# Optimization experiments

Measured on AMD Instinct MI355X. Metric: run time of the kernel, lower is better.

The kernel has to match this reference:

```python
import jax, jax.numpy as jnp
import numpy as np

M_CENTER = 3.0  # diagonal value of the 'centers' matrix
OUT_HW = (513, 513)  # original input spatial size (input_shape in torch forward)


def _conv(x, w, dilation=1, padding=0):
    return jax.lax.conv_general_dilated(
        x, w, window_strides=(1, 1),
        padding=[(padding, padding), (padding, padding)],
        rhs_dilation=(dilation, dilation),
        dimension_numbers=("NCHW", "OIHW", "NCHW"))


def _resize(x, hw):
    return jax.image.resize(x, (x.shape[0], x.shape[1], hw[0], hw[1]), method="bilinear")


def _head(low_level, out, pw, w0, w1, w2, w3, pool_w, aproj_w, cw1, cw2, cb2):
    # DeepLabHeadV3Plus (BN folded to identity at inference: gamma=1, beta=0, mean=0, var=1)
    ll = jax.nn.relu(_conv(low_level, pw))                      # [N,48,129,129]
    branches = [jax.nn.relu(_conv(out, w0))]                    # 1x1 branch
    for w, d in zip((w1, w2, w3), (6, 12, 18)):
        branches.append(jax.nn.relu(_conv(out, w, dilation=d, padding=d)))
    gp = jnp.mean(out, axis=(2, 3), keepdims=True)              # AdaptiveAvgPool2d(1)
    gp = jax.nn.relu(_conv(gp, pool_w))
    gp = jnp.broadcast_to(gp, branches[0].shape)                # bilinear upsample of 1x1 == broadcast
    branches.append(gp)
    y = jax.nn.relu(_conv(jnp.concatenate(branches, axis=1), aproj_w))  # [N,256,33,33]
    y = _resize(y, (ll.shape[2], ll.shape[3]))                  # -> 129x129
    y = jnp.concatenate([ll, y], axis=1)                        # [N,304,129,129]
    y = jax.nn.relu(_conv(y, cw1, padding=1))
    y = _conv(y, cw2) + cb2[None, :, None, None]                # [N,C,129,129]
    return y


def _forward_single(x):
    # x: [N,C,129,129] head logits. Upsample, then squared-distance to diagonal centers (m*I).
    x = _resize(x, OUT_HW)                                      # [N,C,513,513]
    C = x.shape[1]
    features_out = jnp.transpose(x, (0, 2, 3, 1))               # NHWC, as in torch
    # dist2mean[...,c] = -sum_j (f_j - m*1[j==c])^2 = -(|f|^2 - 2*m*f_c + m^2)
    sumsq = jnp.sum(x * x, axis=1, keepdims=True)
    logits = 2.0 * M_CENTER * x - sumsq - M_CENTER * M_CENTER   # [N,C,513,513]
    centers = M_CENTER * jnp.eye(C, dtype=x.dtype)
    return logits, centers, features_out


def _kaiming(key, shape):
    fan_in = shape[1] * shape[2] * shape[3]
    return jax.random.normal(key, shape, jnp.float32) * np.sqrt(2.0 / fan_in)


def _head_params(key, num_classes):
    ks = jax.random.split(key, 10)
    return dict(
        pw=_kaiming(ks[0], (48, 256, 1, 1)),
        w0=_kaiming(ks[1], (256, 2048, 1, 1)),
        w1=_kaiming(ks[2], (256, 2048, 3, 3)),
        w2=_kaiming(ks[3], (256, 2048, 3, 3)),
        w3=_kaiming(ks[4], (256, 2048, 3, 3)),
        pool_w=_kaiming(ks[5], (256, 2048, 1, 1)),
        aproj_w=_kaiming(ks[6], (256, 1280, 1, 1)),
        cw1=_kaiming(ks[7], (256, 304, 3, 3)),
        cw2=_kaiming(ks[8], (num_classes, 256, 1, 1)),
        cb2=jnp.zeros((num_classes,), jnp.float32),
    )


def setup_inputs() -> dict:
    key = jax.random.key(0)
    k_ll, k_out, k_h0, k_h1 = jax.random.split(key, 4)
    inp = {
        "low_level": jax.random.normal(k_ll, (2, 256, 129, 129), jnp.float32),
        "out": jax.random.normal(k_out, (2, 2048, 33, 33), jnp.float32),
    }
    for pref, k, nc in (("h0_", k_h0, 16), ("h1_", k_h1, 17)):
        for name, v in _head_params(k, nc).items():
            inp[pref + name] = v
    return inp


def reference(low_level, out,
              h0_pw, h0_w0, h0_w1, h0_w2, h0_w3, h0_pool_w, h0_aproj_w, h0_cw1, h0_cw2, h0_cb2,
              h1_pw, h1_w0, h1_w1, h1_w2, h1_w3, h1_pool_w, h1_aproj_w, h1_cw1, h1_cw2, h1_cb2):
    x0 = _head(low_level, out, h0_pw, h0_w0, h0_w1, h0_w2, h0_w3, h0_pool_w, h0_aproj_w, h0_cw1, h0_cw2, h0_cb2)
    x1 = _head(low_level, out, h1_pw, h1_w0, h1_w1, h1_w2, h1_w3, h1_pool_w, h1_aproj_w, h1_cw1, h1_cw2, h1_cb2)
    l0, c0, f0 = _forward_single(x0)
    l1, c1, f1 = _forward_single(x1)
    return (l0, l1, c0, c1, f0, f1)
```

## Files before the change

kernel.cpp:

```cpp
#include <hip/hip_runtime.h>

#define TPB 256

typedef _Float16 f16;
typedef __attribute__((ext_vector_type(8))) _Float16 f16x8;
typedef __attribute__((ext_vector_type(16))) float f32x16;

#define GLD_LDS(g, l) __builtin_amdgcn_global_load_lds( \
    (const __attribute__((address_space(1))) void*)(g), \
    (__attribute__((address_space(3))) void*)(l), 16, 0, 0)

__global__ __launch_bounds__(TPB)
void tcz_k(const float* __restrict__ aspp, const float* __restrict__ ll,
           f16* __restrict__ Xa, f16* __restrict__ Xll)
{
    const int bid = blockIdx.x;
    const int tid = threadIdx.x;
    const float* src; f16* dst; int C, HW, ldk, pT, cT, bb;
    if (bid < 4480) {
        src = aspp; dst = Xa; C = 2048; HW = 1089; ldk = 2048;
        pT = bid % 35; cT = (bid / 35) % 64; bb = bid / 2240;
    } else {
        const int b2 = bid - 4480;
        src = ll; dst = Xll; C = 256; HW = 16641; ldk = 256;
        pT = b2 % 521; cT = (b2 / 521) % 8; bb = b2 / 4168;
    }
    __shared__ float t32[32 * 33];
#pragma unroll
    for (int pass = 0; pass < 4; ++pass) {
        const int ch = tid / 32 + pass * 8;
        const int px = tid % 32;
        const int c = cT * 32 + ch, p = pT * 32 + px;
        float v = 0.f;
        if (c < C && p < HW) v = src[((long)bb * C + c) * HW + p];
        t32[ch * 33 + px] = v;
    }
    __syncthreads();
#pragma unroll
    for (int pass = 0; pass < 4; ++pass) {
        const int px = tid / 32 + pass * 8;
        const int ch = tid % 32;
        const int p = pT * 32 + px, c = cT * 32 + ch;
        if (p < HW && c < C)
            dst[((long)bb * HW + p) * ldk + c] = (f16)t32[ch * 33 + px];
    }
}

__global__ __launch_bounds__(TPB)
void tcr_k(const f16* __restrict__ part, f16* __restrict__ dst)
{
    __shared__ float t32[32 * 33];
    const int pT = blockIdx.x, cT = blockIdx.y, bb = blockIdx.z;
    const int tid = threadIdx.x;
    const int br = cT >> 3;
    const f16* pb = part + (long)bb * 2787840;
#pragma unroll
    for (int pass = 0; pass < 4; ++pass) {
        const int ch = tid / 32 + pass * 8;
        const int px = tid % 32;
        const int c = cT * 32 + ch;
        const int cl = c & 255;
        const int p = pT * 32 + px;
        float v = 0.f;
        if (p < 1089) {
            if (br == 0) {
                v = (float)pb[(long)cl * 1089 + p];
            } else {
                const int dl = 6 * br;
                const int y = p / 33;
                const int s0 = 1 + 3 * (br - 1);
#pragma unroll
                for (int g = 0; g < 3; ++g) {
                    const int dy0 = (g - 1) * dl;
                    const int yLo = max(0, -dy0), yHi = min(33, 33 - dy0);
                    if (y >= yLo && y < yHi)
                        v += (float)pb[((long)(s0 + g) * 256 + cl) * 1089 + p];
                }
            }
            v = fmaxf(v, 0.f);
        }
        t32[ch * 33 + px] = v;
    }
    __syncthreads();
#pragma unroll
    for (int pass = 0; pass < 4; ++pass) {
        const int px = tid / 32 + pass * 8;
        const int ch = tid % 32;
        const int p = pT * 32 + px, c = cT * 32 + ch;
        if (p < 1089)
            dst[((long)bb * 1089 + p) * 1024 + c] = (f16)t32[ch * 33 + px];
    }
}

__global__ __launch_bounds__(TPB)
void gpool_k(const float* __restrict__ in, float* __restrict__ gp, int HW, float inv)
{
    const int bc = blockIdx.x;
    const float* p = in + (size_t)bc * HW;
    float s = 0.f;
    for (int i = threadIdx.x; i < HW; i += TPB) s += p[i];
#pragma unroll
    for (int off = 32; off > 0; off >>= 1) s += __shfl_down(s, off, 64);
    __shared__ float red[4];
    if ((threadIdx.x & 63) == 0) red[threadIdx.x >> 6] = s;
    __syncthreads();
    if (threadIdx.x == 0) gp[bc] = (red[0] + red[1] + red[2] + red[3]) * inv;
}

__global__ __launch_bounds__(TPB)
void gemv1_k(const float* __restrict__ pw0, const float* __restrict__ pw1,
             const float* __restrict__ gp, float* __restrict__ gpr2)
{
    const int bh = blockIdx.x & 3;
    const int cgrp = blockIdx.x >> 2;
    const int b = bh & 1;
    const float* w = (bh >> 1) ? pw1 : pw0;
    const int c = cgrp * 16 + (threadIdx.x >> 4);
    const int kl = threadIdx.x & 15;
    const float* g = gp + (size_t)b * 2048;
    float4 acc = {0.f, 0.f, 0.f, 0.f};
    for (int k = kl * 4; k < 2048; k += 64) {
        const float4 wv = *(const float4*)&w[(size_t)c * 2048 + k];
        const float4 gv = *(const float4*)&g[k];
        acc.x = fmaf(wv.x, gv.x, acc.x);
        acc.y = fmaf(wv.y, gv.y, acc.y);
        acc.z = fmaf(wv.z, gv.z, acc.z);
        acc.w = fmaf(wv.w, gv.w, acc.w);
    }
    float s = (acc.x + acc.y) + (acc.z + acc.w);
#pragma unroll
    for (int o = 8; o; o >>= 1) s += __shfl_xor(s, o, 16);
    if (kl == 0) gpr2[bh * 256 + c] = fmaxf(s, 0.f);
}

__global__ __launch_bounds__(TPB)
void gemv2_k(const float* __restrict__ ap0, const float* __restrict__ ap1,
             const float* __restrict__ gpr2, float* __restrict__ gpc2)
{
    const int bh = blockIdx.x & 3;
    const int cgrp = blockIdx.x >> 2;
    const float* w = (bh >> 1) ? ap1 : ap0;
    const int c = cgrp * 16 + (threadIdx.x >> 4);
    const int kl = threadIdx.x & 15;
    const float* g = gpr2 + bh * 256;
    float4 acc = {0.f, 0.f, 0.f, 0.f};
    for (int k = kl * 4; k < 256; k += 64) {
        const float4 wv = *(const float4*)&w[(size_t)c * 1280 + 1024 + k];
        const float4 gv = *(const float4*)&g[k];
        acc.x = fmaf(wv.x, gv.x, acc.x);
        acc.y = fmaf(wv.y, gv.y, acc.y);
        acc.z = fmaf(wv.z, gv.z, acc.z);
        acc.w = fmaf(wv.w, gv.w, acc.w);
    }
    float s = (acc.x + acc.y) + (acc.z + acc.w);
#pragma unroll
    for (int o = 8; o; o >>= 1) s += __shfl_xor(s, o, 16);
    if (kl == 0) gpc2[bh * 256 + c] = s;
}

struct PackJob { const float* w; f16* dst; int Cout, CinUse, CinSrc, T, coP, KB, start; };
struct PackParams { PackJob j[14]; };

__global__ __launch_bounds__(TPB)
void packw_mega(PackParams P, float* __restrict__ guard)
{
    const int bid = blockIdx.x;
    const int tid = threadIdx.x;
    if (bid >= 4832) {
        float4 zv = {0.f, 0.f, 0.f, 0.f};
        float4* p = (float4*)(guard + tid * 16);
        p[0] = zv; p[1] = zv; p[2] = zv; p[3] = zv;
        return;
    }
    int ji = 0;
#pragma unroll
    for (int t = 1; t < 14; ++t) if (bid >= P.j[t].start) ji = t;
    PackJob J;
    switch (ji) {
        case 0:  J = P.j[0];  break;
        case 1:  J = P.j[1];  break;
        case 2:  J = P.j[2];  break;
        case 3:  J = P.j[3];  break;
        case 4:  J = P.j[4];  break;
        case 5:  J = P.j[5];  break;
        case 6:  J = P.j[6];  break;
        case 7:  J = P.j[7];  break;
        case 8:  J = P.j[8];  break;
        case 9:  J = P.j[9];  break;
        case 10: J = P.j[10]; break;
        case 11: J = P.j[11]; break;
        case 12: J = P.j[12]; break;
        default: J = P.j[13]; break;
    }
    const int local = bid - J.start;
    const int kb = local % J.KB;
    const int coT = local / J.KB;
    const int T = J.T;
    __shared__ float tile[16 * 577];
    const int RL = 64 * T;
    const int n = 16 * RL;
    for (int idx = tid; idx < n; idx += TPB) {
        const int row = idx / RL;
        const int jj = idx - row * RL;
        const int co = coT * 16 + row;
        const int k = kb * 64 + jj / T;
        float v = 0.f;
        if (co < J.Cout && k < J.CinUse)
            v = J.w[((long)co * J.CinSrc + kb * 64) * T + jj];
        tile[row * 577 + jj] = v;
    }
    __syncthreads();
    const int nst = 128 * T;
    for (int idx = tid; idx < nst; idx += TPB) {
        const int g = idx & 7;
        const int t = (idx >> 3) % T;
        const int co = idx / (8 * T);
        f16x8 hv;
#pragma unroll
        for (int e = 0; e < 8; ++e)
            hv[e] = (f16)tile[co * 577 + (g * 8 + e) * T + t];
        *(f16x8*)&J.dst[(((long)t * J.KB + kb) * J.coP + coT * 16 + co) * 64 + g * 8] = hv;
    }
}

template <int OUTMODE, int ZMAP, int RELUOUT, int BIAS>
__global__ __launch_bounds__(TPB, 4)
void mconv(const f16* __restrict__ X, const f16* __restrict__ Wp,
           const f16* __restrict__ guard, void* __restrict__ out_,
           const float* __restrict__ gpc,
           int Cinp, int Cout, int H, int W, int kss_, int dl_,
           int kbPerTap, int tapCnt_,
           long xHstr, long wHstr, long oHstr, long outBStride,
           int coP, int ldOut, int NM, int NBH, int NZ)
{
    __shared__ char SH[32768];
    const int tid = threadIdx.x;

    int wg;
    {
        const int orig = blockIdx.x, nwg = gridDim.x;
        const int q = nwg >> 3, r = nwg & 7;
        const int xcd = orig & 7, off = orig >> 3;
        wg = (xcd < r ? xcd * (q + 1) : r * (q + 1) + (xcd - r) * q) + off;
    }
    const int mt = wg % NM; wg /= NM;
    const int bh = wg % NBH; wg /= NBH;
    const int z  = wg % NZ;
    const int nt = wg / NZ;
    const int b = bh & 1, hd = bh >> 1;
    const int co0 = mt * 128;
    const int NP = H * W;
    const long xBstr = (long)NP * Cinp;

    int kss = kss_, dl = dl_, tapStart = 0, tapCnt = tapCnt_;
    long woff = (long)hd * wHstr, ooff = (long)hd * oHstr;
    int p0 = nt * 128, pMax = NP;
    if (ZMAP == 1) {
        int br, grp;
        if (z == 0) { br = 0; grp = 1; kss = 1; dl = 1; tapStart = 0; tapCnt = 1; }
        else { br = 1 + (z - 1) / 3; grp = (z - 1) % 3;
               kss = 3; dl = (br == 1) ? 6 : (br == 2 ? 12 : 18);
               tapStart = grp * 3; tapCnt = 3; }
        woff += (br == 0) ? 0L : (br == 1 ? 524288L : (br == 2 ? 5242880L : 9961472L));
        ooff += (long)z * 278784L;
        const int dy0 = (kss == 1) ? 0 : (grp - 1) * dl;
        const int yLo = max(0, -dy0), yHi = min(H, H - dy0);
        p0 = yLo * W + nt * 128;
        pMax = yHi * W;
        if (p0 >= pMax) return;
    }
    const int half = kss >> 1;
    const int y0t = p0 / W, y1t = min(p0 + 127, pMax - 1) / W;

    int taps[9]; int nval = 0;
    for (int t = 0; t < tapCnt; ++t) {
        const int tp = tapStart + t;
        const int ky = tp / kss;
        const int dy = (ky - half) * dl;
        if (ZMAP == 1 || (y1t + dy >= 0 && y0t + dy < H)) taps[nval++] = tp;
    }
    if (nval == 0) return;

    const int srow = tid >> 3;
    const int sslot = tid & 7;
    int aofs[4];
#pragma unroll
    for (int q = 0; q < 4; ++q) {
        const int row = q * 32 + srow;
        aofs[q] = row * 64 + ((sslot ^ (row & 7)) << 3);
    }
    const long coStr = (long)coP * 64;

    const int lane = tid & 63, wid = tid >> 6;
    const int wm = wid >> 1, wn = wid & 1;
    const int r32 = lane & 31, hh = lane >> 5;
    const int arow0 = wm * 64 + r32, arow1 = arow0 + 32;
    const int brow0 = wn * 64 + r32, brow1 = brow0 + 32;
    const int abase0 = arow0 * 128, abase1 = arow1 * 128;
    const int bbase0 = 16384 + brow0 * 128, bbase1 = 16384 + brow1 * 128;
    const int ax0 = (arow0 & 7), ax1 = (arow1 & 7);
    const int bx0 = (brow0 & 7), bx1 = (brow1 & 7);

    f32x16 acc[2][2];
#pragma unroll
    for (int i = 0; i < 2; ++i)
#pragma unroll
        for (int j = 0; j < 2; ++j) acc[i][j] = (f32x16)(0.f);

    const f16* Pr[4];
    for (int ti = 0; ti < nval; ++ti) {
        const int tp = taps[ti];
        const int ky = tp / kss, kx = tp - ky * kss;
        const int dy = (ky - half) * dl, dx = (kx - half) * dl;
#pragma unroll
        for (int q = 0; q < 4; ++q) {
            const int row = q * 32 + srow;
            const int p = p0 + row;
            bool v = p < pMax;
            const int py = v ? p / W : 0;
            const int px = v ? p - py * W : 0;
            const int sy = py + dy, sx = px + dx;
            v = v && ((unsigned)sy < (unsigned)H) && ((unsigned)sx < (unsigned)W);
            const int swz = (sslot ^ (row & 7)) << 3;
            Pr[q] = v ? (X + (long)b * xBstr + (long)hd * xHstr
                           + ((long)sy * W + sx) * (long)Cinp + swz)
                      : (guard + swz);
        }
        const f16* Wt = Wp + woff + ((long)tp * kbPerTap * coP + (long)co0) * 64;
        for (int kb = 0; kb < kbPerTap; ++kb) {
            __syncthreads();
            const f16* wsrc = Wt + (long)kb * coStr;
            const long kcol = (long)kb << 6;
            GLD_LDS(wsrc + aofs[0], SH + (tid << 4));
            GLD_LDS(wsrc + aofs[1], SH + 4096 + (tid << 4));
            GLD_LDS(wsrc + aofs[2], SH + 8192 + (tid << 4));
            GLD_LDS(wsrc + aofs[3], SH + 12288 + (tid << 4));
            GLD_LDS(Pr[0] + kcol, SH + 16384 + (tid << 4));
            GLD_LDS(Pr[1] + kcol, SH + 20480 + (tid << 4));
            GLD_LDS(Pr[2] + kcol, SH + 24576 + (tid << 4));
            GLD_LDS(Pr[3] + kcol, SH + 28672 + (tid << 4));
            __syncthreads();
            __builtin_amdgcn_s_setprio(1);
#pragma unroll
            for (int kh = 0; kh < 4; ++kh) {
                const int g = kh * 2 + hh;
                const f16x8 a0 = *(const f16x8*)(SH + abase0 + ((g ^ ax0) << 4));
                const f16x8 a1 = *(const f16x8*)(SH + abase1 + ((g ^ ax1) << 4));
                const f16x8 b0 = *(const f16x8*)(SH + bbase0 + ((g ^ bx0) << 4));
                const f16x8 b1 = *(const f16x8*)(SH + bbase1 + ((g ^ bx1) << 4));
                acc[0][0] = __builtin_amdgcn_mfma_f32_32x32x16_f16(a0, b0, acc[0][0], 0, 0, 0);
                acc[0][1] = __builtin_amdgcn_mfma_f32_32x32x16_f16(a0, b1, acc[0][1], 0, 0, 0);
                acc[1][0] = __builtin_amdgcn_mfma_f32_32x32x16_f16(a1, b0, acc[1][0], 0, 0, 0);
                acc[1][1] = __builtin_amdgcn_mfma_f32_32x32x16_f16(a1, b1, acc[1][1], 0, 0, 0);
            }
            __builtin_amdgcn_s_setprio(0);
        }
    }

    const long outB = (long)b * outBStride + ooff;
    const float* gpcp = BIAS ? (gpc + (long)(b + 2 * hd) * 256) : nullptr;
#pragma unroll
    for (int mi = 0; mi < 2; ++mi)
#pragma unroll
    for (int ni = 0; ni < 2; ++ni)
#pragma unroll
    for (int j = 0; j < 16; ++j) {
        const int m = wm * 64 + mi * 32 + 4 * hh + (j & 3) + 8 * (j >> 2);
        const int n = wn * 64 + ni * 32 + r32;
        const int co = co0 + m;
        const int p = p0 + n;
        if (co < Cout && p < pMax) {
            float v = acc[mi][ni][j];
            if (BIAS) v += gpcp[co];
            if (RELUOUT) v = fmaxf(v, 0.f);
            if (OUTMODE == 0)      ((float*)out_)[outB + (long)co * NP + p] = v;
            else if (OUTMODE == 1) ((f16*)out_)[outB + (long)co * NP + p] = (f16)v;
            else if (OUTMODE == 3) ((f16*)out_)[outB + (long)p * ldOut + co] = (f16)v;
            else atomicAdd(&((float*)out_)[outB + (long)co * NP + p], v);
        }
    }
}

__global__ __launch_bounds__(TPB)
void ups2pad_k(const f16* __restrict__ ybx, f16* __restrict__ ccx)
{
    const int idx = blockIdx.x * TPB + threadIdx.x;
    if (idx >= 4 * 16641 * 34) return;
    const int s = idx / (16641 * 34);
    const int rem = idx - s * (16641 * 34);
    const int p = rem / 34;
    const int cg = rem - p * 34;
    if (cg >= 32) {
        f16x8 zv = (f16x8)(f16)0.f;
        *(f16x8*)(ccx + ((long)s * 16641 + p) * 320 + 304 + (cg - 32) * 8) = zv;
        return;
    }
    const int oy = p / 129, ox = p % 129;
    const float sc = 33.0f / 129.0f;
    const float sx = (ox + 0.5f) * sc - 0.5f;
    const float sy = (oy + 0.5f) * sc - 0.5f;
    int ix0 = (int)floorf(sx), iy0 = (int)floorf(sy);
    const float fx = sx - ix0, fy = sy - iy0;
    int ix1 = min(32, max(0, ix0 + 1)); ix0 = min(32, max(0, ix0));
    int iy1 = min(32, max(0, iy0 + 1)); iy0 = min(32, max(0, iy0));
    const f16* base = ybx + (long)s * 1089 * 256 + cg * 8;
    const f16x8 v00 = *(const f16x8*)(base + ((long)iy0 * 33 + ix0) * 256);
    const f16x8 v01 = *(const f16x8*)(base + ((long)iy0 * 33 + ix1) * 256);
    const f16x8 v10 = *(const f16x8*)(base + ((long)iy1 * 33 + ix0) * 256);
    const f16x8 v11 = *(const f16x8*)(base + ((long)iy1 * 33 + ix1) * 256);
    f16x8 r;
#pragma unroll
    for (int e = 0; e < 8; ++e) {
        const float a0 = (float)v00[e] + ((float)v01[e] - (float)v00[e]) * fx;
        const float a1 = (float)v10[e] + ((float)v11[e] - (float)v10[e]) * fx;
        r[e] = (f16)(a0 + (a1 - a0) * fy);
    }
    *(f16x8*)(ccx + ((long)s * 16641 + p) * 320 + 48 + cg * 8) = r;
}

__global__ __launch_bounds__(TPB)
void conv1x1_m(const f16* __restrict__ c1o2,
               const float* __restrict__ w0, const float* __restrict__ w1,
               const float* __restrict__ b0, const float* __restrict__ b1,
               float* __restrict__ xb2)
{
    const int h = blockIdx.z;
    const int nc = h ? 17 : 16;
    const float* w = h ? w1 : w0;
    const float* bias = h ? b1 : b0;
    __shared__ float wsm[256 * 17];
    __shared__ float bsm[17];
    const int tid = threadIdx.x;
    for (int l = tid; l < 256 * 17; l += TPB) {
        const int k = l / 17, c = l - k * 17;
        wsm[l] = (c < nc) ? w[(size_t)c * 256 + k] : 0.f;
    }
    if (tid < nc) bsm[tid] = bias[tid];
    __syncthreads();
    const int b = blockIdx.y;
    const int p = blockIdx.x * TPB + tid;
    if (p >= 16641) return;
    const f16* inB = c1o2 + (long)h * 8520192 + (long)b * 4260096 + p;
    float acc[17];
#pragma unroll
    for (int c = 0; c < 17; ++c) acc[c] = 0.f;
    for (int k = 0; k < 256; ++k) {
        const float x = (float)inB[(size_t)k * 16641];
#pragma unroll
        for (int c = 0; c < 17; ++c) acc[c] = fmaf(wsm[k * 17 + c], x, acc[c]);
    }
    float* oB = xb2 + (h ? 532512L : 0L) + ((long)b * nc) * 16641 + p;
#pragma unroll
    for (int c = 0; c < 17; ++c)
        if (c < nc) oB[(size_t)c * 16641] = acc[c] + bsm[c];
}

__global__ __launch_bounds__(TPB)
void final_m(const float* __restrict__ xb2, float* __restrict__ o)
{
    const int idx = blockIdx.x * TPB + threadIdx.x;
    if (idx >= 2 * 526338) return;
    const int hd = idx / 526338;
    int r = idx - hd * 526338;
    const int ox = r % 513; r /= 513;
    const int oy = r % 513;
    const int b = r / 513;
    const int nc = hd ? 17 : 16;
    const long HW = 513L * 513L;
    const float sc = 129.0f / 513.0f;
    const float sx = (ox + 0.5f) * sc - 0.5f;
    const float sy = (oy + 0.5f) * sc - 0.5f;
    int ix0 = (int)floorf(sx), iy0 = (int)floorf(sy);
    const float fx = sx - ix0, fy = sy - iy0;
    int ix1 = min(128, max(0, ix0 + 1)); ix0 = min(128, max(0, ix0));
    int iy1 = min(128, max(0, iy0 + 1)); iy0 = min(128, max(0, iy0));
    const float* xb = xb2 + (hd ? 532512L : 0L) + (size_t)b * nc * 16641;
    const int i00 = iy0 * 129 + ix0, i01 = iy0 * 129 + ix1;
    const int i10 = iy1 * 129 + ix0, i11 = iy1 * 129 + ix1;
    float* logits = o + (hd ? 8421408L : 0L);
    float* feats  = o + (hd ? 25791107L : 17369699L);
    float v[17];
    float ss = 0.f;
#pragma unroll
    for (int c = 0; c < 17; ++c) {
        if (c < nc) {
            const float* s = xb + (size_t)c * 16641;
            const float a0 = s[i00] + (s[i01] - s[i00]) * fx;
            const float a1 = s[i10] + (s[i11] - s[i10]) * fx;
            const float vv = a0 + (a1 - a0) * fy;
            v[c] = vv;
            ss = fmaf(vv, vv, ss);
        }
    }
    const long pix = (long)oy * 513 + ox;
#pragma unroll
    for (int c = 0; c < 17; ++c)
        if (c < nc)
            logits[((size_t)b * nc + c) * HW + pix] = fmaf(6.f, v[c], -ss - 9.f);
    float* f = feats + ((size_t)b * HW + pix) * nc;
#pragma unroll
    for (int c = 0; c < 17; ++c)
        if (c < nc) f[c] = v[c];
}

__global__ void centers_k(float* __restrict__ c0, float* __restrict__ c1)
{
    const int t = blockIdx.x * 64 + threadIdx.x;
    if (t < 256) c0[t] = (t / 16 == t % 16) ? 3.f : 0.f;
    const int u = t - 256;
    if (u >= 0 && u < 289) c1[u] = (u / 17 == u % 17) ? 3.f : 0.f;
}

extern "C" void kernel_launch(void* const* d_in, const int* in_sizes, int n_in,
                              void* d_out, int out_size, void* d_ws, size_t ws_size,
                              hipStream_t stream)
{
    const float* low_level = (const float*)d_in[0];
    const float* aspp_in   = (const float*)d_in[1];
    float* ws = (float*)d_ws;
    float* o  = (float*)d_out;

    float* GUARDF  = ws + 0;
    f16*   GUARD   = (f16*)GUARDF;
    f16*   Apack2  = (f16*)(ws + 4096);
    f16*   C1O2    = (f16*)(ws + 4096);
    f16*   AprojP2 = (f16*)(ws + 14684160);
    f16*   Cw1P2   = (f16*)(ws + 14946304);
    f16*   LlP2    = (f16*)(ws + 15683584);
    f16*   Xa      = (f16*)(ws + 15716352);
    f16*   BRpart  = (f16*)(ws + 17946624);
    f16*   BRX2    = (f16*)(ws + 23522304);
    f16*   YBX2    = (f16*)(ws + 25752576);
    float* XB2     = ws + 26310144;
    float* GP      = ws + 27408450;
    float* GPC2    = ws + 27412546;
    float* GPR2    = ws + 27413570;

    f16*   CCX2    = (f16*)(o + 0);
    f16*   Xll     = (f16*)(o + 10650240);

    const long C0o = 17369154, C1oo = 17369410;

    tcz_k<<<12816, TPB, 0, stream>>>(aspp_in, low_level, Xa, Xll);
    gpool_k<<<4096, TPB, 0, stream>>>(aspp_in, GP, 1089, 1.0f / 1089.0f);
    gemv1_k<<<64, TPB, 0, stream>>>(
        (const float*)d_in[2 + 5], (const float*)d_in[2 + 10 + 5], GP, GPR2);
    gemv2_k<<<64, TPB, 0, stream>>>(
        (const float*)d_in[2 + 6], (const float*)d_in[2 + 10 + 6], GPR2, GPC2);

    PackParams P;
    int start = 0;
    for (int h = 0; h < 2; ++h) {
        const float* pw    = (const float*)d_in[2 + h * 10 + 0];
        const float* w0    = (const float*)d_in[2 + h * 10 + 1];
        const float* w1    = (const float*)d_in[2 + h * 10 + 2];
        const float* w2    = (const float*)d_in[2 + h * 10 + 3];
        const float* w3    = (const float*)d_in[2 + h * 10 + 4];
        const float* aproj = (const float*)d_in[2 + h * 10 + 6];
        const float* cw1   = (const float*)d_in[2 + h * 10 + 7];
        f16* Ap = Apack2 + (long)h * 14680064;
        const PackJob jobs[7] = {
            { w0,    Ap,                          256, 2048, 2048, 1, 256, 32, 0 },
            { w1,    Ap + 524288,                 256, 2048, 2048, 9, 256, 32, 0 },
            { w2,    Ap + 5242880,                256, 2048, 2048, 9, 256, 32, 0 },
            { w3,    Ap + 9961472,                256, 2048, 2048, 9, 256, 32, 0 },
            { aproj, AprojP2 + (long)h * 262144,  256, 1024, 1280, 1, 256, 16, 0 },
            { cw1,   Cw1P2 + (long)h * 737280,    256,  304,  304, 9, 256,  5, 0 },
            { pw,    LlP2 + (long)h * 32768,       48,  256,  256, 1, 128,  4, 0 },
        };
        for (int t = 0; t < 7; ++t) {
            P.j[h * 7 + t] = jobs[t];
            P.j[h * 7 + t].start = start;
            start += jobs[t].KB * (jobs[t].coP / 16);
        }
    }
    packw_mega<<<4833, TPB, 0, stream>>>(P, GUARDF);

    mconv<1, 1, 0, 0><<<720, TPB, 0, stream>>>(
        Xa, Apack2, GUARD, BRpart, nullptr, 2048, 256, 33, 33, 3, 1,
        32, 0, 0L, 14680064L, 5575680L, 2787840L, 256, 0, 2, 4, 10);
    tcr_k<<<dim3(35, 32, 4), TPB, 0, stream>>>(BRpart, BRX2);
    mconv<3, 0, 1, 1><<<72, TPB, 0, stream>>>(
        BRX2, AprojP2, GUARD, YBX2, GPC2, 1024, 256, 33, 33, 1, 1,
        16, 1, 2230272L, 262144L, 557568L, 278784L, 256, 256, 2, 4, 1);
    mconv<3, 0, 1, 0><<<524, TPB, 0, stream>>>(
        Xll, LlP2, GUARD, CCX2, nullptr, 256, 48, 129, 129, 1, 1,
        4, 1, 0L, 32768L, 10650240L, 5325120L, 128, 320, 1, 4, 1);
    ups2pad_k<<<8841, TPB, 0, stream>>>(YBX2, CCX2);
    mconv<1, 0, 1, 0><<<1048, TPB, 0, stream>>>(
        CCX2, Cw1P2, GUARD, C1O2, nullptr, 320, 256, 129, 129, 3, 1,
        5, 9, 10650240L, 737280L, 8520192L, 4260096L, 256, 0, 2, 4, 1);
    conv1x1_m<<<dim3(66, 2, 2), TPB, 0, stream>>>(C1O2,
        (const float*)d_in[2 + 8], (const float*)d_in[2 + 10 + 8],
        (const float*)d_in[2 + 9], (const float*)d_in[2 + 10 + 9], XB2);
    final_m<<<4113, TPB, 0, stream>>>(XB2, o);
    centers_k<<<9, 64, 0, stream>>>(o + C0o, o + C1oo);
}
```

Before: 637.6 us.

## Split ASPP conv per tap, fuse low-level 1x1 conv and global pool into launches

The dilated ASPP convolution is now split by individual tap (28 z-slices instead of 10), so each workgroup runs 32 K-blocks instead of 96. The low-level 1x1 projection conv is merged into the same launch, and the global-average-pool reduction is folded into the transpose kernel, removing two launches. The aim is more parallelism and fewer launches. The cost is that the partial-sum buffer grows about threefold (moved into the output region) and tcr_k now has to read and sum nine partials per branch instead of three.

```diff
diff --git a/kernel.cpp b/kernel.cpp
--- a/kernel.cpp
+++ b/kernel.cpp
@@ -12,10 +12,24 @@
 
 __global__ __launch_bounds__(TPB)
 void tcz_k(const float* __restrict__ aspp, const float* __restrict__ ll,
-           f16* __restrict__ Xa, f16* __restrict__ Xll)
+           f16* __restrict__ Xa, f16* __restrict__ Xll, float* __restrict__ gp)
 {
     const int bid = blockIdx.x;
     const int tid = threadIdx.x;
+    __shared__ float t32[32 * 33];
+    __shared__ float red[4];
+    if (bid >= 12816) {
+        const int bc = bid - 12816;
+        const float* p = aspp + (size_t)bc * 1089;
+        float s = 0.f;
+        for (int i = tid; i < 1089; i += TPB) s += p[i];
+#pragma unroll
+        for (int off = 32; off > 0; off >>= 1) s += __shfl_down(s, off, 64);
+        if ((tid & 63) == 0) red[tid >> 6] = s;
+        __syncthreads();
+        if (tid == 0) gp[bc] = (red[0] + red[1] + red[2] + red[3]) * (1.0f / 1089.0f);
+        return;
+    }
     const float* src; f16* dst; int C, HW, ldk, pT, cT, bb;
     if (bid < 4480) {
         src = aspp; dst = Xa; C = 2048; HW = 1089; ldk = 2048;
@@ -25,7 +39,6 @@
         src = ll; dst = Xll; C = 256; HW = 16641; ldk = 256;
         pT = b2 % 521; cT = (b2 / 521) % 8; bb = b2 / 4168;
     }
-    __shared__ float t32[32 * 33];
 #pragma unroll
     for (int pass = 0; pass < 4; ++pass) {
         const int ch = tid / 32 + pass * 8;
@@ -53,7 +66,7 @@
     const int pT = blockIdx.x, cT = blockIdx.y, bb = blockIdx.z;
     const int tid = threadIdx.x;
     const int br = cT >> 3;
-    const f16* pb = part + (long)bb * 2787840;
+    const f16* pb = part + (long)bb * 7806464;
 #pragma unroll
     for (int pass = 0; pass < 4; ++pass) {
         const int ch = tid / 32 + pass * 8;
@@ -67,14 +80,14 @@
                 v = (float)pb[(long)cl * 1089 + p];
             } else {
                 const int dl = 6 * br;
+                const int s0 = 1 + 9 * (br - 1);
                 const int y = p / 33;
-                const int s0 = 1 + 3 * (br - 1);
-#pragma unroll
-                for (int g = 0; g < 3; ++g) {
-                    const int dy0 = (g - 1) * dl;
-                    const int yLo = max(0, -dy0), yHi = min(33, 33 - dy0);
+#pragma unroll
+                for (int t = 0; t < 9; ++t) {
+                    const int dy = (t / 3 - 1) * dl;
+                    const int yLo = max(0, -dy), yHi = min(33, 33 - dy);
                     if (y >= yLo && y < yHi)
-                        v += (float)pb[((long)(s0 + g) * 256 + cl) * 1089 + p];
+                        v += (float)pb[((long)(s0 + t) * 256 + cl) * 1089 + p];
                 }
             }
             v = fmaxf(v, 0.f);
@@ -90,21 +103,6 @@
         if (p < 1089)
             dst[((long)bb * 1089 + p) * 1024 + c] = (f16)t32[ch * 33 + px];
     }
-}
-
-__global__ __launch_bounds__(TPB)
-void gpool_k(const float* __restrict__ in, float* __restrict__ gp, int HW, float inv)
-{
-    const int bc = blockIdx.x;
-    const float* p = in + (size_t)bc * HW;
-    float s = 0.f;
-    for (int i = threadIdx.x; i < HW; i += TPB) s += p[i];
-#pragma unroll
-    for (int off = 32; off > 0; off >>= 1) s += __shfl_down(s, off, 64);
-    __shared__ float red[4];
-    if ((threadIdx.x & 63) == 0) red[threadIdx.x >> 6] = s;
-    __syncthreads();
-    if (threadIdx.x == 0) gp[bc] = (red[0] + red[1] + red[2] + red[3]) * inv;
 }
 
 __global__ __launch_bounds__(TPB)
@@ -223,15 +221,11 @@
     }
 }
 
-template <int OUTMODE, int ZMAP, int RELUOUT, int BIAS>
 __global__ __launch_bounds__(TPB, 4)
-void mconv(const f16* __restrict__ X, const f16* __restrict__ Wp,
-           const f16* __restrict__ guard, void* __restrict__ out_,
-           const float* __restrict__ gpc,
-           int Cinp, int Cout, int H, int W, int kss_, int dl_,
-           int kbPerTap, int tapCnt_,
-           long xHstr, long wHstr, long oHstr, long outBStride,
-           int coP, int ldOut, int NM, int NBH, int NZ)
+void mconv2_k(const f16* __restrict__ Xa, const f16* __restrict__ Xll,
+              const f16* __restrict__ Wa, const f16* __restrict__ Wl,
+              const f16* __restrict__ guard, f16* __restrict__ brp,
+              f16* __restrict__ ccx)
 {
     __shared__ char SH[32768];
     const int tid = threadIdx.x;
@@ -243,41 +237,182 @@
         const int xcd = orig & 7, off = orig >> 3;
         wg = (xcd < r ? xcd * (q + 1) : r * (q + 1) + (xcd - r) * q) + off;
     }
+
+    const f16 *X, *Wt;
+    f16* outp;
+    int Cinp, W, NP, kbPerTap, coP, Cout, co0, p0, pMax, dy, dx, H, outmode;
+    long ooff;
+    if (wg < 2016) {
+        const int mt = wg & 1;
+        const int bh = (wg >> 1) & 3;
+        const int z  = (wg >> 3) % 28;
+        const int nt = wg / 224;
+        const int b = bh & 1, hd = bh >> 1;
+        Cinp = 2048; H = 33; W = 33; NP = 1089; kbPerTap = 32;
+        coP = 256; Cout = 256; co0 = mt * 128;
+        int br, tap;
+        if (z == 0) { br = 0; tap = 0; dy = 0; dx = 0; }
+        else {
+            br = 1 + (z - 1) / 9; tap = (z - 1) % 9;
+            const int dl = 6 * br;
+            dy = (tap / 3 - 1) * dl;
+            dx = (tap % 3 - 1) * dl;
+        }
+        const long woff = (long)hd * 14680064L +
+            (br == 0 ? 0L : (br == 1 ? 524288L : (br == 2 ? 5242880L : 9961472L)));
+        Wt = Wa + woff + ((long)tap * 32 * 256 + co0) * 64;
+        X = Xa + (long)b * (1089L * 2048);
+        const int yLo = max(0, -dy), yHi = min(33, 33 - dy);
+        p0 = yLo * 33 + nt * 128;
+        pMax = yHi * 33;
+        if (p0 >= pMax) return;
+        outp = brp;
+        ooff = (long)(2 * hd + b) * 7806464L + (long)z * 278784L;
+        outmode = 1;
+    } else {
+        const int local = wg - 2016;
+        const int bh = local & 3;
+        const int nt = local >> 2;
+        const int b = bh & 1, hd = bh >> 1;
+        Cinp = 256; H = 129; W = 129; NP = 16641; kbPerTap = 4;
+        coP = 128; Cout = 48; co0 = 0;
+        dy = 0; dx = 0;
+        p0 = nt * 128; pMax = 16641;
+        if (p0 >= pMax) return;
+        X = Xll + (long)b * (16641L * 256);
+        Wt = Wl + (long)hd * 32768L;
+        outp = ccx;
+        ooff = (long)(2 * hd + b) * 5325120L;
+        outmode = 3;
+    }
+
+    const int srow = tid >> 3;
+    const int sslot = tid & 7;
+    int aofs[4];
+#pragma unroll
+    for (int q = 0; q < 4; ++q) {
+        const int row = q * 32 + srow;
+        aofs[q] = row * 64 + ((sslot ^ (row & 7)) << 3);
+    }
+    const f16* Pr[4];
+#pragma unroll
+    for (int q = 0; q < 4; ++q) {
+        const int row = q * 32 + srow;
+        const int p = p0 + row;
+        bool v = p < pMax;
+        const int py = v ? p / W : 0;
+        const int px = v ? p - py * W : 0;
+        const int sy = py + dy, sx = px + dx;
+        v = v && ((unsigned)sy < (unsigned)H) && ((unsigned)sx < (unsigned)W);
+        const int swz = (sslot ^ (row & 7)) << 3;
+        Pr[q] = v ? (X + ((long)sy * W + sx) * Cinp + swz) : (guard + swz);
+    }
+    const long coStr = (long)coP * 64;
+
+    const int lane = tid & 63, wid = tid >> 6;
+    const int wm = wid >> 1, wn = wid & 1;
+    const int r32 = lane & 31, hh = lane >> 5;
+    const int arow0 = wm * 64 + r32, arow1 = arow0 + 32;
+    const int brow0 = wn * 64 + r32, brow1 = brow0 + 32;
+    const int abase0 = arow0 * 128, abase1 = arow1 * 128;
+    const int bbase0 = 16384 + brow0 * 128, bbase1 = 16384 + brow1 * 128;
+    const int ax0 = (arow0 & 7), ax1 = (arow1 & 7);
+    const int bx0 = (brow0 & 7), bx1 = (brow1 & 7);
+
+    f32x16 acc[2][2];
+#pragma unroll
+    for (int i = 0; i < 2; ++i)
+#pragma unroll
+        for (int j = 0; j < 2; ++j) acc[i][j] = (f32x16)(0.f);
+
+    for (int kb = 0; kb < kbPerTap; ++kb) {
+        __syncthreads();
+        const f16* wsrc = Wt + (long)kb * coStr;
+        const long kcol = (long)kb << 6;
+        GLD_LDS(wsrc + aofs[0], SH + (tid << 4));
+        GLD_LDS(wsrc + aofs[1], SH + 4096 + (tid << 4));
+        GLD_LDS(wsrc + aofs[2], SH + 8192 + (tid << 4));
+        GLD_LDS(wsrc + aofs[3], SH + 12288 + (tid << 4));
+        GLD_LDS(Pr[0] + kcol, SH + 16384 + (tid << 4));
+        GLD_LDS(Pr[1] + kcol, SH + 20480 + (tid << 4));
+        GLD_LDS(Pr[2] + kcol, SH + 24576 + (tid << 4));
+        GLD_LDS(Pr[3] + kcol, SH + 28672 + (tid << 4));
+        __syncthreads();
+        __builtin_amdgcn_s_setprio(1);
+#pragma unroll
+        for (int kh = 0; kh < 4; ++kh) {
+            const int g = kh * 2 + hh;
+            const f16x8 a0 = *(const f16x8*)(SH + abase0 + ((g ^ ax0) << 4));
+            const f16x8 a1 = *(const f16x8*)(SH + abase1 + ((g ^ ax1) << 4));
+            const f16x8 b0 = *(const f16x8*)(SH + bbase0 + ((g ^ bx0) << 4));
+            const f16x8 b1 = *(const f16x8*)(SH + bbase1 + ((g ^ bx1) << 4));
+            acc[0][0] = __builtin_amdgcn_mfma_f32_32x32x16_f16(a0, b0, acc[0][0], 0, 0, 0);
+            acc[0][1] = __builtin_amdgcn_mfma_f32_32x32x16_f16(a0, b1, acc[0][1], 0, 0, 0);
+            acc[1][0] = __builtin_amdgcn_mfma_f32_32x32x16_f16(a1, b0, acc[1][0], 0, 0, 0);
+            acc[1][1] = __builtin_amdgcn_mfma_f32_32x32x16_f16(a1, b1, acc[1][1], 0, 0, 0);
+        }
+        __builtin_amdgcn_s_setprio(0);
+    }
+
+#pragma unroll
+    for (int mi = 0; mi < 2; ++mi)
+#pragma unroll
+    for (int ni = 0; ni < 2; ++ni)
+#pragma unroll
+    for (int j = 0; j < 16; ++j) {
+        const int m = wm * 64 + mi * 32 + 4 * hh + (j & 3) + 8 * (j >> 2);
+        const int n = wn * 64 + ni * 32 + r32;
+        const int co = co0 + m;
+        const int p = p0 + n;
+        if (co < Cout && p < pMax) {
+            const float v = acc[mi][ni][j];
+            if (outmode == 1)
+                outp[ooff + (long)co * NP + p] = (f16)v;
+            else
+                outp[ooff + (long)p * 320 + co] = (f16)fmaxf(v, 0.f);
+        }
+    }
+}
+
+template <int OUTMODE, int RELUOUT, int BIAS>
+__global__ __launch_bounds__(TPB, 4)
+void mconv(const f16* __restrict__ X, const f16* __restrict__ Wp,
+           const f16* __restrict__ guard, void* __restrict__ out_,
+           const float* __restrict__ gpc,
+           int Cinp, int Cout, int H, int W, int kss, int dl,
+           int kbPerTap, int tapCnt,
+           long xHstr, long wHstr, long oHstr, long outBStride,
+           int coP, int ldOut, int NM, int NBH, int NZ)
+{
+    __shared__ char SH[32768];
+    const int tid = threadIdx.x;
+
+    int wg;
+    {
+        const int orig = blockIdx.x, nwg = gridDim.x;
+        const int q = nwg >> 3, r = nwg & 7;
+        const int xcd = orig & 7, off = orig >> 3;
+        wg = (xcd < r ? xcd * (q + 1) : r * (q + 1) + (xcd - r) * q) + off;
+    }
     const int mt = wg % NM; wg /= NM;
     const int bh = wg % NBH; wg /= NBH;
-    const int z  = wg % NZ;
     const int nt = wg / NZ;
     const int b = bh & 1, hd = bh >> 1;
     const int co0 = mt * 128;
     const int NP = H * W;
     const long xBstr = (long)NP * Cinp;
 
-    int kss = kss_, dl = dl_, tapStart = 0, tapCnt = tapCnt_;
-    long woff = (long)hd * wHstr, ooff = (long)hd * oHstr;
-    int p0 = nt * 128, pMax = NP;
-    if (ZMAP == 1) {
-        int br, grp;
-        if (z == 0) { br = 0; grp = 1; kss = 1; dl = 1; tapStart = 0; tapCnt = 1; }
-        else { br = 1 + (z - 1) / 3; grp = (z - 1) % 3;
-               kss = 3; dl = (br == 1) ? 6 : (br == 2 ? 12 : 18);
-               tapStart = grp * 3; tapCnt = 3; }
-        woff += (br == 0) ? 0L : (br == 1 ? 524288L : (br == 2 ? 5242880L : 9961472L));
-        ooff += (long)z * 278784L;
-        const int dy0 = (kss == 1) ? 0 : (grp - 1) * dl;
-        const int yLo = max(0, -dy0), yHi = min(H, H - dy0);
-        p0 = yLo * W + nt * 128;
-        pMax = yHi * W;
-        if (p0 >= pMax) return;
-    }
+    const long woff = (long)hd * wHstr, ooff = (long)hd * oHstr;
+    const int p0 = nt * 128, pMax = NP;
+    if (p0 >= pMax) return;
     const int half = kss >> 1;
     const int y0t = p0 / W, y1t = min(p0 + 127, pMax - 1) / W;
 
     int taps[9]; int nval = 0;
     for (int t = 0; t < tapCnt; ++t) {
-        const int tp = tapStart + t;
-        const int ky = tp / kss;
-        const int dy = (ky - half) * dl;
-        if (ZMAP == 1 || (y1t + dy >= 0 && y0t + dy < H)) taps[nval++] = tp;
+        const int ky = t / kss;
+        const int dyv = (ky - half) * dl;
+        if (y1t + dyv >= 0 && y0t + dyv < H) taps[nval++] = t;
     }
     if (nval == 0) return;
 
@@ -373,10 +508,8 @@
             float v = acc[mi][ni][j];
             if (BIAS) v += gpcp[co];
             if (RELUOUT) v = fmaxf(v, 0.f);
-            if (OUTMODE == 0)      ((float*)out_)[outB + (long)co * NP + p] = v;
-            else if (OUTMODE == 1) ((f16*)out_)[outB + (long)co * NP + p] = (f16)v;
-            else if (OUTMODE == 3) ((f16*)out_)[outB + (long)p * ldOut + co] = (f16)v;
-            else atomicAdd(&((float*)out_)[outB + (long)co * NP + p], v);
+            if (OUTMODE == 1) ((f16*)out_)[outB + (long)co * NP + p] = (f16)v;
+            else              ((f16*)out_)[outB + (long)p * ldOut + co] = (f16)v;
         }
     }
 }
@@ -528,21 +661,20 @@
     f16*   Cw1P2   = (f16*)(ws + 14946304);
     f16*   LlP2    = (f16*)(ws + 15683584);
     f16*   Xa      = (f16*)(ws + 15716352);
-    f16*   BRpart  = (f16*)(ws + 17946624);
-    f16*   BRX2    = (f16*)(ws + 23522304);
-    f16*   YBX2    = (f16*)(ws + 25752576);
-    float* XB2     = ws + 26310144;
-    float* GP      = ws + 27408450;
-    float* GPC2    = ws + 27412546;
-    float* GPR2    = ws + 27413570;
+    f16*   BRX2    = (f16*)(ws + 17946624);
+    f16*   YBX2    = (f16*)(ws + 20176896);
+    float* XB2     = ws + 20734464;
+    float* GP      = ws + 21832770;
+    float* GPC2    = ws + 21836866;
+    float* GPR2    = ws + 21837890;
 
     f16*   CCX2    = (f16*)(o + 0);
     f16*   Xll     = (f16*)(o + 10650240);
+    f16*   BRpart  = (f16*)(o + 14910336);
 
     const long C0o = 17369154, C1oo = 17369410;
 
-    tcz_k<<<12816, TPB, 0, stream>>>(aspp_in, low_level, Xa, Xll);
-    gpool_k<<<4096, TPB, 0, stream>>>(aspp_in, GP, 1089, 1.0f / 1089.0f);
+    tcz_k<<<16912, TPB, 0, stream>>>(aspp_in, low_level, Xa, Xll, GP);
     gemv1_k<<<64, TPB, 0, stream>>>(
         (const float*)d_in[2 + 5], (const float*)d_in[2 + 10 + 5], GP, GPR2);
     gemv2_k<<<64, TPB, 0, stream>>>(
@@ -576,18 +708,13 @@
     }
     packw_mega<<<4833, TPB, 0, stream>>>(P, GUARDF);
 
-    mconv<1, 1, 0, 0><<<720, TPB, 0, stream>>>(
-        Xa, Apack2, GUARD, BRpart, nullptr, 2048, 256, 33, 33, 3, 1,
-        32, 0, 0L, 14680064L, 5575680L, 2787840L, 256, 0, 2, 4, 10);
+    mconv2_k<<<2540, TPB, 0, stream>>>(Xa, Xll, Apack2, LlP2, GUARD, BRpart, CCX2);
     tcr_k<<<dim3(35, 32, 4), TPB, 0, stream>>>(BRpart, BRX2);
-    mconv<3, 0, 1, 1><<<72, TPB, 0, stream>>>(
+    mconv<3, 1, 1><<<72, TPB, 0, stream>>>(
         BRX2, AprojP2, GUARD, YBX2, GPC2, 1024, 256, 33, 33, 1, 1,
         16, 1, 2230272L, 262144L, 557568L, 278784L, 256, 256, 2, 4, 1);
-    mconv<3, 0, 1, 0><<<524, TPB, 0, stream>>>(
-        Xll, LlP2, GUARD, CCX2, nullptr, 256, 48, 129, 129, 1, 1,
-        4, 1, 0L, 32768L, 10650240L, 5325120L, 128, 320, 1, 4, 1);
     ups2pad_k<<<8841, TPB, 0, stream>>>(YBX2, CCX2);
-    mconv<1, 0, 1, 0><<<1048, TPB, 0, stream>>>(
+    mconv<1, 1, 0><<<1048, TPB, 0, stream>>>(
         CCX2, Cw1P2, GUARD, C1O2, nullptr, 320, 256, 129, 129, 3, 1,
         5, 9, 10650240L, 737280L, 8520192L, 4260096L, 256, 0, 2, 4, 1);
     conv1x1_m<<<dim3(66, 2, 2), TPB, 0, stream>>>(C1O2,
```

Result: slower. 666.1 us (+4.5%).

## Double-buffer LDS in mconv and fold global pooling into transpose kernel

Applied to the files above, without the earlier changes.

The implicit-GEMM conv kernel now keeps two 32KB LDS stages, issuing global-to-LDS loads for the next K-step before running MFMAs on the current one. A flattened tap/kb step loop with explicit vmcnt waits and barriers replaces the nested loop, and launch bounds drop to 2 blocks per CU to fit the doubled shared memory. The global average pool kernel is merged into the transpose kernel as extra blocks, saving one launch. Unused output modes (fp32 store and atomics) are removed from the epilogue. The cost is lower occupancy, which may hurt latency hiding in exchange for the overlap.

```diff
diff --git a/kernel.cpp b/kernel.cpp
--- a/kernel.cpp
+++ b/kernel.cpp
@@ -12,10 +12,24 @@
 
 __global__ __launch_bounds__(TPB)
 void tcz_k(const float* __restrict__ aspp, const float* __restrict__ ll,
-           f16* __restrict__ Xa, f16* __restrict__ Xll)
+           f16* __restrict__ Xa, f16* __restrict__ Xll, float* __restrict__ gp)
 {
     const int bid = blockIdx.x;
     const int tid = threadIdx.x;
+    __shared__ float t32[32 * 33];
+    __shared__ float red[4];
+    if (bid >= 12816) {
+        const int bc = bid - 12816;
+        const float* p = aspp + (size_t)bc * 1089;
+        float s = 0.f;
+        for (int i = tid; i < 1089; i += TPB) s += p[i];
+#pragma unroll
+        for (int off = 32; off > 0; off >>= 1) s += __shfl_down(s, off, 64);
+        if ((tid & 63) == 0) red[tid >> 6] = s;
+        __syncthreads();
+        if (tid == 0) gp[bc] = (red[0] + red[1] + red[2] + red[3]) * (1.0f / 1089.0f);
+        return;
+    }
     const float* src; f16* dst; int C, HW, ldk, pT, cT, bb;
     if (bid < 4480) {
         src = aspp; dst = Xa; C = 2048; HW = 1089; ldk = 2048;
@@ -25,7 +39,6 @@
         src = ll; dst = Xll; C = 256; HW = 16641; ldk = 256;
         pT = b2 % 521; cT = (b2 / 521) % 8; bb = b2 / 4168;
     }
-    __shared__ float t32[32 * 33];
 #pragma unroll
     for (int pass = 0; pass < 4; ++pass) {
         const int ch = tid / 32 + pass * 8;
@@ -90,21 +103,6 @@
         if (p < 1089)
             dst[((long)bb * 1089 + p) * 1024 + c] = (f16)t32[ch * 33 + px];
     }
-}
-
-__global__ __launch_bounds__(TPB)
-void gpool_k(const float* __restrict__ in, float* __restrict__ gp, int HW, float inv)
-{
-    const int bc = blockIdx.x;
-    const float* p = in + (size_t)bc * HW;
-    float s = 0.f;
-    for (int i = threadIdx.x; i < HW; i += TPB) s += p[i];
-#pragma unroll
-    for (int off = 32; off > 0; off >>= 1) s += __shfl_down(s, off, 64);
-    __shared__ float red[4];
-    if ((threadIdx.x & 63) == 0) red[threadIdx.x >> 6] = s;
-    __syncthreads();
-    if (threadIdx.x == 0) gp[bc] = (red[0] + red[1] + red[2] + red[3]) * inv;
 }
 
 __global__ __launch_bounds__(TPB)
@@ -224,7 +222,7 @@
 }
 
 template <int OUTMODE, int ZMAP, int RELUOUT, int BIAS>
-__global__ __launch_bounds__(TPB, 4)
+__global__ __launch_bounds__(TPB, 2)
 void mconv(const f16* __restrict__ X, const f16* __restrict__ Wp,
            const f16* __restrict__ guard, void* __restrict__ out_,
            const float* __restrict__ gpc,
@@ -233,7 +231,7 @@
            long xHstr, long wHstr, long oHstr, long outBStride,
            int coP, int ldOut, int NM, int NBH, int NZ)
 {
-    __shared__ char SH[32768];
+    __shared__ char SH[65536];
     const int tid = threadIdx.x;
 
     int wg;
@@ -280,6 +278,7 @@
         if (ZMAP == 1 || (y1t + dy >= 0 && y0t + dy < H)) taps[nval++] = tp;
     }
     if (nval == 0) return;
+    const int nSteps = nval * kbPerTap;
 
     const int srow = tid >> 3;
     const int sslot = tid & 7;
@@ -291,25 +290,11 @@
     }
     const long coStr = (long)coP * 64;
 
-    const int lane = tid & 63, wid = tid >> 6;
-    const int wm = wid >> 1, wn = wid & 1;
-    const int r32 = lane & 31, hh = lane >> 5;
-    const int arow0 = wm * 64 + r32, arow1 = arow0 + 32;
-    const int brow0 = wn * 64 + r32, brow1 = brow0 + 32;
-    const int abase0 = arow0 * 128, abase1 = arow1 * 128;
-    const int bbase0 = 16384 + brow0 * 128, bbase1 = 16384 + brow1 * 128;
-    const int ax0 = (arow0 & 7), ax1 = (arow1 & 7);
-    const int bx0 = (brow0 & 7), bx1 = (brow1 & 7);
-
-    f32x16 acc[2][2];
-#pragma unroll
-    for (int i = 0; i < 2; ++i)
-#pragma unroll
-        for (int j = 0; j < 2; ++j) acc[i][j] = (f32x16)(0.f);
-
+    int cTi = 0, cKb = 0;
+    const f16* Wt;
     const f16* Pr[4];
-    for (int ti = 0; ti < nval; ++ti) {
-        const int tp = taps[ti];
+    auto refresh = [&]() {
+        const int tp = taps[cTi];
         const int ky = tp / kss, kx = tp - ky * kss;
         const int dy = (ky - half) * dl, dx = (kx - half) * dl;
 #pragma unroll
@@ -326,35 +311,71 @@
                            + ((long)sy * W + sx) * (long)Cinp + swz)
                       : (guard + swz);
         }
-        const f16* Wt = Wp + woff + ((long)tp * kbPerTap * coP + (long)co0) * 64;
-        for (int kb = 0; kb < kbPerTap; ++kb) {
-            __syncthreads();
-            const f16* wsrc = Wt + (long)kb * coStr;
-            const long kcol = (long)kb << 6;
-            GLD_LDS(wsrc + aofs[0], SH + (tid << 4));
-            GLD_LDS(wsrc + aofs[1], SH + 4096 + (tid << 4));
-            GLD_LDS(wsrc + aofs[2], SH + 8192 + (tid << 4));
-            GLD_LDS(wsrc + aofs[3], SH + 12288 + (tid << 4));
-            GLD_LDS(Pr[0] + kcol, SH + 16384 + (tid << 4));
-            GLD_LDS(Pr[1] + kcol, SH + 20480 + (tid << 4));
-            GLD_LDS(Pr[2] + kcol, SH + 24576 + (tid << 4));
-            GLD_LDS(Pr[3] + kcol, SH + 28672 + (tid << 4));
-            __syncthreads();
-            __builtin_amdgcn_s_setprio(1);
-#pragma unroll
-            for (int kh = 0; kh < 4; ++kh) {
-                const int g = kh * 2 + hh;
-                const f16x8 a0 = *(const f16x8*)(SH + abase0 + ((g ^ ax0) << 4));
-                const f16x8 a1 = *(const f16x8*)(SH + abase1 + ((g ^ ax1) << 4));
-                const f16x8 b0 = *(const f16x8*)(SH + bbase0 + ((g ^ bx0) << 4));
-                const f16x8 b1 = *(const f16x8*)(SH + bbase1 + ((g ^ bx1) << 4));
-                acc[0][0] = __builtin_amdgcn_mfma_f32_32x32x16_f16(a0, b0, acc[0][0], 0, 0, 0);
-                acc[0][1] = __builtin_amdgcn_mfma_f32_32x32x16_f16(a0, b1, acc[0][1], 0, 0, 0);
-                acc[1][0] = __builtin_amdgcn_mfma_f32_32x32x16_f16(a1, b0, acc[1][0], 0, 0, 0);
-                acc[1][1] = __builtin_amdgcn_mfma_f32_32x32x16_f16(a1, b1, acc[1][1], 0, 0, 0);
-            }
-            __builtin_amdgcn_s_setprio(0);
+        Wt = Wp + woff + ((long)tp * kbPerTap * coP + (long)co0) * 64;
+    };
+    auto stageTo = [&](char* base) {
+        const f16* wsrc = Wt + (long)cKb * coStr;
+        const long kcol = (long)cKb << 6;
+        GLD_LDS(wsrc + aofs[0], base + (tid << 4));
+        GLD_LDS(wsrc + aofs[1], base + 4096 + (tid << 4));
+        GLD_LDS(wsrc + aofs[2], base + 8192 + (tid << 4));
+        GLD_LDS(wsrc + aofs[3], base + 12288 + (tid << 4));
+        GLD_LDS(Pr[0] + kcol, base + 16384 + (tid << 4));
+        GLD_LDS(Pr[1] + kcol, base + 20480 + (tid << 4));
+        GLD_LDS(Pr[2] + kcol, base + 24576 + (tid << 4));
+        GLD_LDS(Pr[3] + kcol, base + 28672 + (tid << 4));
+    };
+    auto adv = [&]() {
+        if (++cKb == kbPerTap) { cKb = 0; if (++cTi < nval) refresh(); }
+    };
+
+    const int lane = tid & 63, wid = tid >> 6;
+    const int wm = wid >> 1, wn = wid & 1;
+    const int r32 = lane & 31, hh = lane >> 5;
+    const int arow0 = wm * 64 + r32, arow1 = arow0 + 32;
+    const int brow0 = wn * 64 + r32, brow1 = brow0 + 32;
+    const int abase0 = arow0 * 128, abase1 = arow1 * 128;
+    const int bbase0 = 16384 + brow0 * 128, bbase1 = 16384 + brow1 * 128;
+    const int ax0 = (arow0 & 7), ax1 = (arow1 & 7);
+    const int bx0 = (brow0 & 7), bx1 = (brow1 & 7);
+
+    f32x16 acc[2][2];
+#pragma unroll
+    for (int i = 0; i < 2; ++i)
+#pragma unroll
+        for (int j = 0; j < 2; ++j) acc[i][j] = (f32x16)(0.f);
+
+    refresh();
+    stageTo(SH);
+    adv();
+
+    for (int s = 0; s < nSteps; ++s) {
+        char* cbuf = SH + (s & 1) * 32768;
+        if (s + 1 < nSteps) {
+            stageTo(SH + ((s + 1) & 1) * 32768);
+            adv();
+            asm volatile("s_waitcnt vmcnt(8)" ::: "memory");
+        } else {
+            asm volatile("s_waitcnt vmcnt(0)" ::: "memory");
         }
+        __builtin_amdgcn_s_barrier();
+        __builtin_amdgcn_sched_barrier(0);
+        __builtin_amdgcn_s_setprio(1);
+#pragma unroll
+        for (int kh = 0; kh < 4; ++kh) {
+            const int g = kh * 2 + hh;
+            const f16x8 a0 = *(const f16x8*)(cbuf + abase0 + ((g ^ ax0) << 4));
+            const f16x8 a1 = *(const f16x8*)(cbuf + abase1 + ((g ^ ax1) << 4));
+            const f16x8 b0 = *(const f16x8*)(cbuf + bbase0 + ((g ^ bx0) << 4));
+            const f16x8 b1 = *(const f16x8*)(cbuf + bbase1 + ((g ^ bx1) << 4));
+            acc[0][0] = __builtin_amdgcn_mfma_f32_32x32x16_f16(a0, b0, acc[0][0], 0, 0, 0);
+            acc[0][1] = __builtin_amdgcn_mfma_f32_32x32x16_f16(a0, b1, acc[0][1], 0, 0, 0);
+            acc[1][0] = __builtin_amdgcn_mfma_f32_32x32x16_f16(a1, b0, acc[1][0], 0, 0, 0);
+            acc[1][1] = __builtin_amdgcn_mfma_f32_32x32x16_f16(a1, b1, acc[1][1], 0, 0, 0);
+        }
+        __builtin_amdgcn_s_setprio(0);
+        __builtin_amdgcn_sched_barrier(0);
+        __builtin_amdgcn_s_barrier();
     }
 
     const long outB = (long)b * outBStride + ooff;
@@ -373,10 +394,8 @@
             float v = acc[mi][ni][j];
             if (BIAS) v += gpcp[co];
             if (RELUOUT) v = fmaxf(v, 0.f);
-            if (OUTMODE == 0)      ((float*)out_)[outB + (long)co * NP + p] = v;
-            else if (OUTMODE == 1) ((f16*)out_)[outB + (long)co * NP + p] = (f16)v;
-            else if (OUTMODE == 3) ((f16*)out_)[outB + (long)p * ldOut + co] = (f16)v;
-            else atomicAdd(&((float*)out_)[outB + (long)co * NP + p], v);
+            if (OUTMODE == 1) ((f16*)out_)[outB + (long)co * NP + p] = (f16)v;
+            else              ((f16*)out_)[outB + (long)p * ldOut + co] = (f16)v;
         }
     }
 }
@@ -541,8 +560,7 @@
 
     const long C0o = 17369154, C1oo = 17369410;
 
-    tcz_k<<<12816, TPB, 0, stream>>>(aspp_in, low_level, Xa, Xll);
-    gpool_k<<<4096, TPB, 0, stream>>>(aspp_in, GP, 1089, 1.0f / 1089.0f);
+    tcz_k<<<16912, TPB, 0, stream>>>(aspp_in, low_level, Xa, Xll, GP);
     gemv1_k<<<64, TPB, 0, stream>>>(
         (const float*)d_in[2 + 5], (const float*)d_in[2 + 10 + 5], GP, GPR2);
     gemv2_k<<<64, TPB, 0, stream>>>(
```

Result: slower. 653.2 us (+2.4%).
